# Optimization experiments

Measured on AMD Instinct MI355X. Metric: run time of the kernel, lower is better.

The kernel has to match this reference:

```python
import jax, jax.numpy as jnp
import numpy as np
import math

H = 12   # num_attention_heads
DH = 64  # attention_head_size
D = H * DH  # hidden_size = 768


def _split_heads(x):
    # [b, s, D] -> [b, H, s, DH]
    b, s, _ = x.shape
    return x.reshape(b, s, H, DH).transpose(0, 2, 1, 3)


def setup_inputs() -> dict:
    key = jax.random.key(0)
    ks = jax.random.split(key, 8)
    B, S, G, NUM_CTX = 32, 512, 16, 8
    real_b = B // NUM_CTX
    inp = {
        "hidden_states": jax.random.normal(ks[0], (B, S, D), dtype=jnp.float32),
        "attention_mask": jnp.zeros((B, 1, 1, S), dtype=jnp.float32),
        "global_tokens_embed": jax.random.normal(ks[1], (real_b, G, D), dtype=jnp.float32),
        "Wq": jax.random.normal(ks[2], (D, D), dtype=jnp.float32) * 0.02,
        "bq": jnp.zeros((D,), dtype=jnp.float32),
        "Wk": jax.random.normal(ks[3], (D, D), dtype=jnp.float32) * 0.02,
        "bk": jnp.zeros((D,), dtype=jnp.float32),
        "Wv": jax.random.normal(ks[4], (D, D), dtype=jnp.float32) * 0.02,
        "bv": jnp.zeros((D,), dtype=jnp.float32),
        "num_ctx": 8,
    }
    return inp


def reference(hidden_states, attention_mask, global_tokens_embed,
              Wq, bq, Wk, bk, Wv, bv, num_ctx):
    B, S, _ = hidden_states.shape
    real_b = B // num_ctx
    G = global_tokens_embed.shape[1]
    scale = 1.0 / math.sqrt(DH)

    # Q/K/V projections for packed contexts
    q = _split_heads(hidden_states @ Wq + bq)   # [B,H,S,DH]
    k = _split_heads(hidden_states @ Wk + bk)
    v = _split_heads(hidden_states @ Wv + bv)

    # Global token projections
    gq = _split_heads(global_tokens_embed @ Wq + bq)  # [real_b,H,G,DH]
    gk = _split_heads(global_tokens_embed @ Wk + bk)
    gv = _split_heads(global_tokens_embed @ Wv + bv)

    # ---- Global-token cross attention over all contexts of each real batch ----
    # [B,H,S,DH] -> [real_b, H, num_ctx*S, DH]
    full_k = k.transpose(0, 2, 1, 3).reshape(real_b, num_ctx * S, H, DH).transpose(0, 2, 1, 3)
    full_v = v.transpose(0, 2, 1, 3).reshape(real_b, num_ctx * S, H, DH).transpose(0, 2, 1, 3)
    full_k = jnp.concatenate([gk, full_k], axis=2)  # [real_b,H,G+num_ctx*S,DH]
    full_v = jnp.concatenate([gv, full_v], axis=2)

    g_scores = jnp.einsum('bhgd,bhkd->bhgk', gq, full_k) * scale
    g_mask = attention_mask.reshape(real_b, num_ctx * S)[:, None, None, :]
    g_mask = jnp.concatenate([jnp.zeros((real_b, 1, 1, G), g_mask.dtype), g_mask], axis=3)
    g_scores = g_scores + g_mask
    g_probs = jax.nn.softmax(g_scores, axis=-1)
    g_ctx = jnp.einsum('bhgk,bhkd->bhgd', g_probs, full_v)
    g_ctx = g_ctx.transpose(0, 2, 1, 3).reshape(real_b, G, D)  # [real_b,G,D]

    # ---- Local attention: each context attends to its own tokens + global tokens ----
    gk_rep = jnp.broadcast_to(gk[:, None], (real_b, num_ctx, H, G, DH)).reshape(B, H, G, DH)
    gv_rep = jnp.broadcast_to(gv[:, None], (real_b, num_ctx, H, G, DH)).reshape(B, H, G, DH)
    k2 = jnp.concatenate([gk_rep, k], axis=2)  # [B,H,G+S,DH]
    v2 = jnp.concatenate([gv_rep, v], axis=2)
    mask2 = jnp.concatenate([jnp.zeros((B, 1, 1, G), attention_mask.dtype), attention_mask], axis=3)

    scores = jnp.einsum('bhqd,bhkd->bhqk', q, k2) * scale + mask2  # [B,H,S,G+S]
    probs = jax.nn.softmax(scores, axis=-1)
    ctx = jnp.einsum('bhqk,bhkd->bhqd', probs, v2)
    ctx = ctx.transpose(0, 2, 1, 3).reshape(B, S, D)  # [B,S,D]

    return ctx, g_ctx
```

## Files before the change

### kernel.cpp

```cpp
#include <hip/hip_runtime.h>
#include <hip/hip_bf16.h>
#include <stdint.h>

#define NH 12
#define DHD 64
#define DM 768
#define BB 32
#define SS 512
#define GG 16
#define NCTX 8
#define RBATCH 4
#define OUTG_OFF ((size_t)BB * SS * DM)

#define XROWS 16512
#define NALL 2304
#define NX8 (XROWS * DM / 8)
#define NB8 (NALL / 8)
#define NM8 (BB * SS / 8)

#define LOG2E 1.4426950408889634f
#define QSCALE 0.18033688011112042f

typedef __bf16 bf16x8 __attribute__((ext_vector_type(8)));
typedef float f32x4 __attribute__((ext_vector_type(4)));
typedef float f32x16 __attribute__((ext_vector_type(16)));

__device__ __forceinline__ float b2f(unsigned short u) {
    union { unsigned int i; float f; } x;
    x.i = ((unsigned int)u) << 16;
    return x.f;
}
__device__ __forceinline__ unsigned short f2b(float f) {
    __hip_bfloat16 h = __float2bfloat16(f);
    return *reinterpret_cast<unsigned short*>(&h);
}
__device__ __forceinline__ unsigned int pk2(float a, float b) {
    return ((unsigned int)f2b(b) << 16) | (unsigned int)f2b(a);
}
__device__ __forceinline__ float ex2(float x) {
    return __builtin_amdgcn_exp2f(x);
}
__device__ __forceinline__ float ldv(const void* p, size_t i, int isf32) {
    return isf32 ? ((const float*)p)[i] : b2f(((const unsigned short*)p)[i]);
}
__device__ __forceinline__ void stv(void* p, size_t i, int isf32, float v) {
    if (isf32) ((float*)p)[i] = v;
    else       ((unsigned short*)p)[i] = f2b(v);
}
__device__ __forceinline__ void async_cp16(const unsigned short* g, unsigned short* l) {
    __builtin_amdgcn_global_load_lds(
        (const __attribute__((address_space(1))) unsigned int*)g,
        (__attribute__((address_space(3))) unsigned int*)l, 16, 0, 0);
}

__device__ __forceinline__ void vt_pair_store(unsigned int* Vt32, int vr, int scc,
                                              uint4 a, uint4 b, int ldq) {
    const unsigned int* au = (const unsigned int*)&a;
    const unsigned int* bu = (const unsigned int*)&b;
    #pragma unroll
    for (int i = 0; i < 4; i++) {
        const int d0 = scc + 2 * i;
        const int swz = ((vr >> 3) ^ ((d0 >> 3) & 7));
        const int i32 = d0 * ldq + (swz << 2) + ((vr & 7) >> 1);
        Vt32[i32]       = __builtin_amdgcn_perm(bu[i], au[i], 0x05040100u);
        Vt32[i32 + ldq] = __builtin_amdgcn_perm(bu[i], au[i], 0x07060302u);
    }
}

__global__ __launch_bounds__(256) void detect_dtype(
    const unsigned short* __restrict__ Wq, int* __restrict__ flag)
{
    __shared__ int hi, zz;
    if (threadIdx.x == 0) { hi = 0; zz = 0; }
    __syncthreads();
    int lh = 0, lz = 0;
    for (int i = threadIdx.x; i < 4096; i += 256) {
        unsigned short u = Wq[2 * i];
        if (((u >> 7) & 0xFF) >= 130) lh++;
        if (u == 0) lz++;
    }
    atomicAdd(&hi, lh);
    atomicAdd(&zz, lz);
    __syncthreads();
    if (threadIdx.x == 0) *flag = (hi > 512 || zz > 3500) ? 1 : 0;
}

__global__ __launch_bounds__(256) void cvt_x(
    const void* __restrict__ hs, const void* __restrict__ gte,
    const void* __restrict__ bq, const void* __restrict__ bk,
    const void* __restrict__ bv, const void* __restrict__ mask,
    const int* __restrict__ flag,
    unsigned short* __restrict__ Xb, unsigned short* __restrict__ b_all,
    unsigned short* __restrict__ wmask)
{
    const int e = blockIdx.x * 256 + threadIdx.x;
    const int isf32 = *flag;
    if (e < NX8) {
        const int base = e * 8;
        const int row = base / DM, col = base % DM;
        unsigned short o8[8];
        if (row < 16384) {
            if (isf32) {
                float4 a = ((const float4*)hs)[e * 2];
                float4 c = ((const float4*)hs)[e * 2 + 1];
                o8[0]=f2b(a.x); o8[1]=f2b(a.y); o8[2]=f2b(a.z); o8[3]=f2b(a.w);
                o8[4]=f2b(c.x); o8[5]=f2b(c.y); o8[6]=f2b(c.z); o8[7]=f2b(c.w);
            } else {
                *(uint4*)o8 = ((const uint4*)hs)[e];
            }
        } else if (row < 16448) {
            size_t soff = (size_t)(row - 16384) * DM + col;
            #pragma unroll
            for (int i = 0; i < 8; i++) o8[i] = f2b(ldv(gte, soff + i, isf32));
        } else {
            #pragma unroll
            for (int i = 0; i < 8; i++) o8[i] = 0;
        }
        *(uint4*)&Xb[base] = *(const uint4*)o8;
    } else if (e < NX8 + NB8) {
        const int i0 = (e - NX8) * 8;
        #pragma unroll
        for (int i = 0; i < 8; i++) {
            int ng = i0 + i;
            int z = ng / DM;
            const void* src = (z == 0) ? bq : (z == 1) ? bk : bv;
            b_all[ng] = f2b(ldv(src, ng % DM, isf32));
        }
    } else if (e < NX8 + NB8 + NM8) {
        const int i0 = (e - NX8 - NB8) * 8;
        #pragma unroll
        for (int i = 0; i < 8; i++)
            wmask[i0 + i] = f2b(ldv(mask, i0 + i, isf32) * LOG2E);
    }
}

__global__ __launch_bounds__(256) void cvt_w(
    const void* __restrict__ Wq, const void* __restrict__ Wk,
    const void* __restrict__ Wv, const int* __restrict__ flag,
    unsigned short* __restrict__ Wt)
{
    __shared__ float T[64][65];
    const int kt = blockIdx.x;
    const int ngt = blockIdx.y;
    const int z = ngt / 12, nt = ngt % 12;
    const int tid = threadIdx.x;
    const int isf32 = *flag;
    const void* W = (z == 0) ? Wq : (z == 1) ? Wk : Wv;

    for (int jj = 0; jj < 16; jj++) {
        int el = tid + jj * 256;
        int r = el >> 6, c = el & 63;
        T[r][c] = ldv(W, (size_t)(kt * 64 + r) * DM + nt * 64 + c, isf32);
    }
    __syncthreads();
    for (int jj = 0; jj < 16; jj++) {
        int el = tid + jj * 256;
        int rn = el >> 6, ck = el & 63;
        Wt[(size_t)(z * DM + nt * 64 + rn) * DM + kt * 64 + ck] = f2b(T[ck][rn]);
    }
}

__global__ __launch_bounds__(256) void qkv_gemm(
    const unsigned short* __restrict__ Xb,
    const unsigned short* __restrict__ Wt,
    const unsigned short* __restrict__ b_all,
    unsigned short* __restrict__ q, unsigned short* __restrict__ kk_,
    unsigned short* __restrict__ v,
    unsigned short* __restrict__ gq, unsigned short* __restrict__ gk,
    unsigned short* __restrict__ gv)
{
    __shared__ __align__(16) unsigned short As[128 * 32];
    __shared__ __align__(16) unsigned short Bs[128 * 32];

    const int mt = blockIdx.x, nt = blockIdx.y;
    const int tid = threadIdx.x;
    const int wave = tid >> 6, lane = tid & 63;
    const int quad = lane >> 4, l16 = lane & 15;
    const int wm = wave & 1, wn = wave >> 1;
    const int z = nt / 6;
    unsigned short* YL = (z == 0) ? q : (z == 1) ? kk_ : v;
    unsigned short* YG = (z == 0) ? gq : (z == 1) ? gk : gv;
    const float qsc = (z == 0) ? QSCALE : 1.0f;

    const int sr = tid >> 2, sc = (tid & 3) * 8;

    f32x4 acc[4][4];
    #pragma unroll
    for (int i = 0; i < 4; i++)
        for (int j = 0; j < 4; j++)
            for (int r = 0; r < 4; r++) acc[i][j][r] = 0.f;

    for (int k0 = 0; k0 < DM; k0 += 32) {
        __syncthreads();
        async_cp16(&Xb[(size_t)(mt * 128 + sr) * DM + k0 + sc], &As[wave * 512]);
        async_cp16(&Xb[(size_t)(mt * 128 + 64 + sr) * DM + k0 + sc], &As[2048 + wave * 512]);
        async_cp16(&Wt[(size_t)(nt * 128 + sr) * DM + k0 + sc], &Bs[wave * 512]);
        async_cp16(&Wt[(size_t)(nt * 128 + 64 + sr) * DM + k0 + sc], &Bs[2048 + wave * 512]);
        __syncthreads();

        bf16x8 af[4], bf[4];
        #pragma unroll
        for (int ib = 0; ib < 4; ib++)
            af[ib] = *(const bf16x8*)&As[(wm * 64 + ib * 16 + l16) * 32 + quad * 8];
        #pragma unroll
        for (int jb = 0; jb < 4; jb++)
            bf[jb] = *(const bf16x8*)&Bs[(wn * 64 + jb * 16 + l16) * 32 + quad * 8];
        #pragma unroll
        for (int ib = 0; ib < 4; ib++)
            #pragma unroll
            for (int jb = 0; jb < 4; jb++)
                acc[ib][jb] = __builtin_amdgcn_mfma_f32_16x16x32_bf16(
                    af[ib], bf[jb], acc[ib][jb], 0, 0, 0);
    }

    #pragma unroll
    for (int jb = 0; jb < 4; jb++) {
        const int ng = nt * 128 + wn * 64 + jb * 16 + l16;
        const float bias = b2f(b_all[ng]);
        const int o = ng - z * DM;
        const int h = o >> 6, dh = o & 63;
        #pragma unroll
        for (int ib = 0; ib < 4; ib++) {
            #pragma unroll
            for (int r = 0; r < 4; r++) {
                const int m = mt * 128 + wm * 64 + ib * 16 + quad * 4 + r;
                const unsigned short ob = f2b((acc[ib][jb][r] + bias) * qsc);
                if (m < 16384) {
                    const int b = m >> 9, s = m & 511;
                    YL[(((size_t)b * NH + h) * SS + s) * DHD + dh] = ob;
                } else if (m < 16448) {
                    const int gl = m - 16384;
                    const int rbx = gl >> 4, g = gl & 15;
                    YG[(((size_t)rbx * NH + h) * GG + g) * DHD + dh] = ob;
                }
            }
        }
    }
}

__global__ __launch_bounds__(256) void attn_local(
    const unsigned short* __restrict__ q,
    const unsigned short* __restrict__ k,
    const unsigned short* __restrict__ v,
    const unsigned short* __restrict__ gk,
    const unsigned short* __restrict__ gv,
    const unsigned short* __restrict__ wmask,
    const int* __restrict__ flag,
    void* __restrict__ out)
{
    __shared__ __align__(16) unsigned short Ks[64 * 64];
    __shared__ __align__(16) unsigned short Vt[64 * 64];

    const int qt = blockIdx.x, h = blockIdx.y, b = blockIdx.z;
    const int rb = b >> 3;
    const int tid = threadIdx.x, wave = tid >> 6, lane = tid & 63;
    const int l31 = lane & 31, h8 = lane >> 5;
    const int isf32 = *flag;
    const int q0 = qt * 128 + wave * 32;

    const size_t bh = (size_t)b * NH + h;
    const unsigned short* qp = q + bh * SS * DHD;
    const unsigned short* kp = k + bh * SS * DHD;
    const unsigned short* vp = v + bh * SS * DHD;
    const size_t gbh = (size_t)rb * NH + h;
    const unsigned short* gkp = gk + gbh * GG * DHD;
    const unsigned short* gvp = gv + gbh * GG * DHD;

    bf16x8 qf[4];
    #pragma unroll
    for (int kb = 0; kb < 4; kb++)
        qf[kb] = *(const bf16x8*)&qp[(size_t)(q0 + l31) * DHD + kb * 16 + h8 * 8];

    f32x16 oacc[2];
    #pragma unroll
    for (int mb = 0; mb < 2; mb++)
        #pragma unroll
        for (int j = 0; j < 16; j++) oacc[mb][j] = 0.f;
    float m_s = -1e30f, l_s = 0.f;

    const int sr = tid >> 3, scc = (tid & 7) * 8;
    const int vr = sr * 2;
    const int agc = (((lane & 7) ^ ((lane >> 3) & 7)) << 3);
    const int arow = 8 * wave + (lane >> 3);
    unsigned int* Vt32 = (unsigned int*)Vt;

    for (int t = 0; t < 9; t++) {
        __syncthreads();
        if (t == 0) {
            if (sr < 16) {
                uint4 kx = *(const uint4*)&gkp[sr * DHD + scc];
                *(uint4*)&Ks[sr * 64 + (((scc >> 3) ^ (sr & 7)) << 3)] = kx;
            } else {
                uint4 zz4 = {0, 0, 0, 0};
                *(uint4*)&Ks[sr * 64 + (((scc >> 3) ^ (sr & 7)) << 3)] = zz4;
            }
            uint4 va = {0, 0, 0, 0}, vb = {0, 0, 0, 0};
            if (sr < 8) {
                va = *(const uint4*)&gvp[vr * DHD + scc];
                vb = *(const uint4*)&gvp[(vr + 1) * DHD + scc];
            }
            vt_pair_store(Vt32, vr, scc, va, vb, 32);
        } else {
            const int ks0 = (t - 1) * 64;
            #pragma unroll
            for (int p = 0; p < 2; p++)
                async_cp16(&kp[(size_t)(ks0 + p * 32 + arow) * DHD + agc],
                           &Ks[p * 2048 + wave * 512]);
            uint4 va = *(const uint4*)&vp[(size_t)(ks0 + vr) * DHD + scc];
            uint4 vb = *(const uint4*)&vp[(size_t)(ks0 + vr + 1) * DHD + scc];
            vt_pair_store(Vt32, vr, scc, va, vb, 32);
        }
        __syncthreads();

        f32x16 scA, scB;
        #pragma unroll
        for (int kt = 0; kt < 2; kt++) {
            f32x16 cc;
            #pragma unroll
            for (int j = 0; j < 16; j++) cc[j] = 0.f;
            if (kt == 0 || t > 0) {
                #pragma unroll
                for (int kb = 0; kb < 4; kb++) {
                    const int key = kt * 32 + l31;
                    bf16x8 kf = *(const bf16x8*)&Ks[key * 64 + (((kb * 2 + h8) ^ (key & 7)) << 3)];
                    cc = __builtin_amdgcn_mfma_f32_32x32x16_bf16(kf, qf[kb], cc, 0, 0, 0);
                }
                if (t > 0) {
                    #pragma unroll
                    for (int rg = 0; rg < 4; rg++) {
                        uint2 mu = *(const uint2*)&wmask[b * SS + (t - 1) * 64 + kt * 32 + rg * 8 + 4 * h8];
                        const unsigned short* mp = (const unsigned short*)&mu;
                        #pragma unroll
                        for (int r = 0; r < 4; r++)
                            cc[rg * 4 + r] += b2f(mp[r]);
                    }
                } else {
                    #pragma unroll
                    for (int j = 8; j < 16; j++) cc[j] = -1e30f;
                }
            } else {
                #pragma unroll
                for (int j = 0; j < 16; j++) cc[j] = -1e30f;
            }
            if (kt == 0) scA = cc; else scB = cc;
        }

        float mx = -1e30f;
        #pragma unroll
        for (int j = 0; j < 16; j++) mx = fmaxf(mx, scA[j]);
        #pragma unroll
        for (int j = 0; j < 16; j++) mx = fmaxf(mx, scB[j]);
        mx = fmaxf(mx, __shfl_xor(mx, 32, 64));
        if (!__all(mx <= m_s)) {
            const float mn = fmaxf(m_s, mx);
            const float alpha = ex2(m_s - mn);
            m_s = mn;
            l_s *= alpha;
            #pragma unroll
            for (int mb = 0; mb < 2; mb++)
                #pragma unroll
                for (int j = 0; j < 16; j++) oacc[mb][j] *= alpha;
        }
        float rs = 0.f;
        #pragma unroll
        for (int j = 0; j < 16; j++) { float pw = ex2(scA[j] - m_s); scA[j] = pw; rs += pw; }
        #pragma unroll
        for (int j = 0; j < 16; j++) { float pw = ex2(scB[j] - m_s); scB[j] = pw; rs += pw; }
        rs += __shfl_xor(rs, 32, 64);
        l_s += rs;

        #pragma unroll
        for (int kt = 0; kt < 2; kt++) {
            unsigned int wA[4], wB[4];
            #pragma unroll
            for (int g = 0; g < 4; g++) {
                const float s0 = (kt == 0) ? scA[4 * g + 0] : scB[4 * g + 0];
                const float s1 = (kt == 0) ? scA[4 * g + 1] : scB[4 * g + 1];
                const float s2 = (kt == 0) ? scA[4 * g + 2] : scB[4 * g + 2];
                const float s3 = (kt == 0) ? scA[4 * g + 3] : scB[4 * g + 3];
                wA[g] = pk2(s0, s1);
                wB[g] = pk2(s2, s3);
            }
            #pragma unroll
            for (int kb = 0; kb < 2; kb++) {
                auto ra  = __builtin_amdgcn_permlane32_swap(wA[2 * kb], wA[2 * kb + 1], false, false);
                auto rbp = __builtin_amdgcn_permlane32_swap(wB[2 * kb], wB[2 * kb + 1], false, false);
                union { unsigned int u[4]; bf16x8 v8; } pfu;
                pfu.u[0] = (unsigned int)ra[0];
                pfu.u[1] = (unsigned int)rbp[0];
                pfu.u[2] = (unsigned int)ra[1];
                pfu.u[3] = (unsigned int)rbp[1];
                const int kb2 = kt * 2 + kb;
                #pragma unroll
                for (int mb = 0; mb < 2; mb++) {
                    const int d = mb * 32 + l31;
                    bf16x8 vf = *(const bf16x8*)&Vt[d * 64 + (((kb2 * 2 + h8) ^ ((d >> 3) & 7)) << 3)];
                    oacc[mb] = __builtin_amdgcn_mfma_f32_32x32x16_bf16(vf, pfu.v8, oacc[mb], 0, 0, 0);
                }
            }
        }
    }

    const float inv = 1.f / l_s;
    const int s = q0 + l31;
    #pragma unroll
    for (int mb = 0; mb < 2; mb++) {
        #pragma unroll
        for (int rg = 0; rg < 4; rg++) {
            const int d0 = mb * 32 + rg * 8 + 4 * h8;
            const size_t idx = ((size_t)b * SS + s) * DM + h * DHD + d0;
            if (isf32) {
                float4 o4;
                o4.x = oacc[mb][rg * 4 + 0] * inv;
                o4.y = oacc[mb][rg * 4 + 1] * inv;
                o4.z = oacc[mb][rg * 4 + 2] * inv;
                o4.w = oacc[mb][rg * 4 + 3] * inv;
                *(float4*)&((float*)out)[idx] = o4;
            } else {
                uint2 o2;
                o2.x = pk2(oacc[mb][rg * 4 + 0] * inv, oacc[mb][rg * 4 + 1] * inv);
                o2.y = pk2(oacc[mb][rg * 4 + 2] * inv, oacc[mb][rg * 4 + 3] * inv);
                *(uint2*)&((unsigned short*)out)[idx] = o2;
            }
        }
    }
}

__global__ __launch_bounds__(256) void attn_gsplit(
    const unsigned short* __restrict__ k,
    const unsigned short* __restrict__ v,
    const unsigned short* __restrict__ gq,
    const unsigned short* __restrict__ gk,
    const unsigned short* __restrict__ gv,
    const unsigned short* __restrict__ wmask,
    float* __restrict__ Opart, float* __restrict__ Mpart,
    float* __restrict__ Lpart)
{
    __shared__ __align__(16) unsigned short Ks[128 * 64];
    __shared__ __align__(16) unsigned short Vt[64 * 128];
    __shared__ __align__(16) unsigned short Ps[4 * 16 * 64];

    const int h = blockIdx.x, rb = blockIdx.y, sp = blockIdx.z;
    const int tid = threadIdx.x, wave = tid >> 6, lane = tid & 63;
    const int quad = lane >> 4, l16 = lane & 15;

    const size_t gbh = (size_t)rb * NH + h;
    const unsigned short* gqp = gq + gbh * GG * DHD;
    const unsigned short* gkp = gk + gbh * GG * DHD;
    const unsigned short* gvp = gv + gbh * GG * DHD;

    bf16x8 aq[2];
    aq[0] = *(const bf16x8*)&gqp[l16 * DHD + quad * 8];
    aq[1] = *(const bf16x8*)&gqp[l16 * DHD + 32 + quad * 8];

    f32x4 oacc[4];
    #pragma unroll
    for (int db = 0; db < 4; db++)
        for (int r = 0; r < 4; r++) oacc[db][r] = 0.f;
    float m_s = -1e30f, l_s = 0.f;

    const int sr = tid >> 3, scc = (tid & 7) * 8;
    const int vr = sr * 2;
    const int agc = (((lane & 7) ^ ((lane >> 3) & 7)) << 3);
    const int arow = 8 * wave + (lane >> 3);
    unsigned short* myP = &Ps[wave * 1024];
    unsigned int* Vt32 = (unsigned int*)Vt;

    const int nt = (sp == 0) ? 9 : 8;
    for (int ti = 0; ti < nt; ti++) {
        const bool gtile = (sp == 0 && ti == 0);
        int cb = 0, soff = 0;
        __syncthreads();
        if (gtile) {
            if (sr < 16) {
                uint4 kx = *(const uint4*)&gkp[sr * DHD + scc];
                *(uint4*)&Ks[sr * 64 + (((scc >> 3) ^ (sr & 7)) << 3)] = kx;
                uint4 va = {0, 0, 0, 0}, vb = {0, 0, 0, 0};
                if (sr < 8) {
                    va = *(const uint4*)&gvp[vr * DHD + scc];
                    vb = *(const uint4*)&gvp[(vr + 1) * DHD + scc];
                }
                vt_pair_store(Vt32, vr, scc, va, vb, 64);
            } else {
                uint4 zz4 = {0, 0, 0, 0};
                *(uint4*)&Ks[sr * 64 + (((scc >> 3) ^ (sr & 7)) << 3)] = zz4;
            }
        } else {
            const int kidx = sp * 1024 + (ti - ((sp == 0) ? 1 : 0)) * 128;
            cb = rb * NCTX + (kidx >> 9);
            soff = kidx & 511;
            const unsigned short* kp = k + ((size_t)cb * NH + h) * SS * DHD;
            const unsigned short* vp = v + ((size_t)cb * NH + h) * SS * DHD;
            #pragma unroll
            for (int p = 0; p < 4; p++)
                async_cp16(&kp[(size_t)(soff + p * 32 + arow) * DHD + agc],
                           &Ks[p * 2048 + wave * 512]);
            #pragma unroll
            for (int pp = 0; pp < 2; pp++) {
                const int vrr = vr + pp * 64;
                uint4 va = *(const uint4*)&vp[(size_t)(soff + vrr) * DHD + scc];
                uint4 vb = *(const uint4*)&vp[(size_t)(soff + vrr + 1) * DHD + scc];
                vt_pair_store(Vt32, vrr, scc, va, vb, 64);
            }
        }
        __syncthreads();

        if (gtile && wave != 0) continue;

        const int nbn = gtile ? 1 : 2;
        f32x4 c[2];
        for (int hh = 0; hh < nbn; hh++) {
            f32x4 cc = {0.f, 0.f, 0.f, 0.f};
            const int key = wave * 32 + hh * 16 + l16;
            #pragma unroll
            for (int kd = 0; kd < 2; kd++) {
                bf16x8 kf = *(const bf16x8*)&Ks[key * 64 + (((kd * 4 + quad) ^ (key & 7)) << 3)];
                cc = __builtin_amdgcn_mfma_f32_16x16x32_bf16(kf, aq[kd], cc, 0, 0, 0);
            }
            if (!gtile) {
                uint2 mu = *(const uint2*)&wmask[cb * SS + soff + wave * 32 + hh * 16 + quad * 4];
                const unsigned short* mp = (const unsigned short*)&mu;
                #pragma unroll
                for (int r = 0; r < 4; r++)
                    cc[r] += b2f(mp[r]);
            }
            c[hh] = cc;
        }

        float mx = -1e30f;
        for (int hh = 0; hh < nbn; hh++)
            #pragma unroll
            for (int r = 0; r < 4; r++) mx = fmaxf(mx, c[hh][r]);
        mx = fmaxf(mx, __shfl_xor(mx, 16, 64));
        mx = fmaxf(mx, __shfl_xor(mx, 32, 64));
        const float mn = fmaxf(m_s, mx);
        const float alpha = ex2(m_s - mn);
        m_s = mn;
        float rs = 0.f;
        for (int hh = 0; hh < nbn; hh++)
            #pragma unroll
            for (int r = 0; r < 4; r++) {
                float p = ex2(c[hh][r] - mn);
                c[hh][r] = p;
                rs += p;
            }
        rs += __shfl_xor(rs, 16, 64);
        rs += __shfl_xor(rs, 32, 64);
        l_s = l_s * alpha + rs;
        #pragma unroll
        for (int db = 0; db < 4; db++)
            for (int r = 0; r < 4; r++) oacc[db][r] *= alpha;

        for (int hh = 0; hh < nbn; hh++) {
            uint2 pw;
            pw.x = pk2(c[hh][0], c[hh][1]);
            pw.y = pk2(c[hh][2], c[hh][3]);
            const int cch = ((hh * 2 + (quad >> 1)) ^ (l16 & 7));
            *(uint2*)&myP[l16 * 64 + cch * 8 + (quad & 1) * 4] = pw;
        }
        if (nbn == 1) {
            uint2 zz2; zz2.x = 0; zz2.y = 0;
            const int cch = ((2 + (quad >> 1)) ^ (l16 & 7));
            *(uint2*)&myP[l16 * 64 + cch * 8 + (quad & 1) * 4] = zz2;
        }

        bf16x8 pf = *(const bf16x8*)&myP[l16 * 64 + ((quad ^ (l16 & 7)) << 3)];
        #pragma unroll
        for (int db = 0; db < 4; db++) {
            const int d = db * 16 + l16;
            const int kc = wave * 4 + quad;
            bf16x8 vf = *(const bf16x8*)&Vt[d * 128 + ((kc ^ ((d >> 3) & 7)) << 3)];
            oacc[db] = __builtin_amdgcn_mfma_f32_16x16x32_bf16(vf, pf, oacc[db], 0, 0, 0);
        }
    }

    __syncthreads();
    float* Om = (float*)Ks;
    float* Mw = (float*)Vt;
    float* Lw = Mw + 64;
    #pragma unroll
    for (int db = 0; db < 4; db++)
        for (int r = 0; r < 4; r++)
            Om[(wave * 16 + l16) * 64 + db * 16 + quad * 4 + r] = oacc[db][r];
    if (quad == 0) {
        Mw[wave * 16 + l16] = m_s;
        Lw[wave * 16 + l16] = l_s;
    }
    __syncthreads();

    const size_t pbase = ((size_t)(sp * RBATCH + rb) * NH + h) * 1024;
    for (int e = tid; e < 1024; e += 256) {
        const int qrow = e >> 6, d = e & 63;
        float M = fmaxf(fmaxf(Mw[qrow], Mw[16 + qrow]), fmaxf(Mw[32 + qrow], Mw[48 + qrow]));
        float acc = 0.f, L = 0.f;
        #pragma unroll
        for (int w = 0; w < 4; w++) {
            float scw = ex2(Mw[w * 16 + qrow] - M);
            acc += Om[(w * 16 + qrow) * 64 + d] * scw;
            L += Lw[w * 16 + qrow] * scw;
        }
        Opart[pbase + e] = acc;
        if (d == 0) {
            Mpart[((sp * RBATCH + rb) * NH + h) * 16 + qrow] = M;
            Lpart[((sp * RBATCH + rb) * NH + h) * 16 + qrow] = L;
        }
    }
}

__global__ __launch_bounds__(256) void attn_gmerge(
    const float* __restrict__ Opart, const float* __restrict__ Mpart,
    const float* __restrict__ Lpart, const int* __restrict__ flag,
    void* __restrict__ out)
{
    const int h = blockIdx.x, rb = blockIdx.y;
    const int tid = threadIdx.x;
    const int isf32 = *flag;
    for (int e = tid; e < 1024; e += 256) {
        const int qrow = e >> 6, d = e & 63;
        float M = -1e30f;
        #pragma unroll
        for (int sp = 0; sp < 4; sp++)
            M = fmaxf(M, Mpart[((sp * RBATCH + rb) * NH + h) * 16 + qrow]);
        float acc = 0.f, L = 0.f;
        #pragma unroll
        for (int sp = 0; sp < 4; sp++) {
            const size_t pb = ((size_t)(sp * RBATCH + rb) * NH + h);
            float scs = ex2(Mpart[pb * 16 + qrow] - M);
            acc += Opart[pb * 1024 + e] * scs;
            L += Lpart[pb * 16 + qrow] * scs;
        }
        stv(out, OUTG_OFF + ((size_t)rb * GG + qrow) * DM + h * DHD + d, isf32, acc / L);
    }
}

extern "C" void kernel_launch(void* const* d_in, const int* in_sizes, int n_in,
                              void* d_out, int out_size, void* d_ws, size_t ws_size,
                              hipStream_t stream) {
    const void* hs   = d_in[0];
    const void* mask = d_in[1];
    const void* gte  = d_in[2];
    const void* Wq   = d_in[3];
    const void* bq   = d_in[4];
    const void* Wk   = d_in[5];
    const void* bk   = d_in[6];
    const void* Wv   = d_in[7];
    const void* bv   = d_in[8];

    const size_t qkv_sz = (size_t)BB * NH * SS * DHD;
    const size_t g_sz   = (size_t)RBATCH * NH * GG * DHD;
    const size_t msk_sz = (size_t)BB * SS;
    const size_t x_sz   = (size_t)XROWS * DM;
    const size_t wt_sz  = (size_t)NALL * DM;
    const size_t ba_sz  = (size_t)NALL;
    const size_t need_hw = 3 * qkv_sz + 3 * g_sz + msk_sz + x_sz + wt_sz + ba_sz;
    if (ws_size < need_hw * 2 + 16) return;

    unsigned short* q     = (unsigned short*)d_ws;
    unsigned short* kk    = q + qkv_sz;
    unsigned short* vv    = kk + qkv_sz;
    unsigned short* gq    = vv + qkv_sz;
    unsigned short* gk    = gq + g_sz;
    unsigned short* gv    = gk + g_sz;
    unsigned short* wmask = gv + g_sz;
    unsigned short* Xb    = wmask + msk_sz;
    unsigned short* Wt    = Xb + x_sz;
    unsigned short* b_all = Wt + wt_sz;
    int* flag = (int*)(b_all + ba_sz);
    float* Opart = (float*)Xb;
    float* Mpart = Opart + 4 * RBATCH * NH * 1024;
    float* Lpart = Mpart + 4 * RBATCH * NH * 16;

    detect_dtype<<<1, 256, 0, stream>>>((const unsigned short*)Wq, flag);

    const int cvt_items = NX8 + NB8 + NM8;
    cvt_x<<<(cvt_items + 255) / 256, 256, 0, stream>>>(
        hs, gte, bq, bk, bv, mask, flag, Xb, b_all, wmask);
    cvt_w<<<dim3(12, 36), 256, 0, stream>>>(Wq, Wk, Wv, flag, Wt);

    qkv_gemm<<<dim3(129, 18), 256, 0, stream>>>(Xb, Wt, b_all, q, kk, vv, gq, gk, gv);

    attn_local<<<dim3(4, NH, BB), 256, 0, stream>>>(
        q, kk, vv, gk, gv, wmask, flag, d_out);
    attn_gsplit<<<dim3(NH, RBATCH, 4), 256, 0, stream>>>(
        kk, vv, gq, gk, gv, wmask, Opart, Mpart, Lpart);
    attn_gmerge<<<dim3(NH, RBATCH), 256, 0, stream>>>(
        Opart, Mpart, Lpart, flag, d_out);
}
```

Before: 360.5 us.

## Double-buffer QKV GEMM, swizzle blocks across XCDs, vectorize epilogue stores

The QKV GEMM now double-buffers its LDS tiles, so the async copies for the next K-slice are issued while MFMAs run on the current one, and it needs one barrier per iteration instead of two. Both the GEMM and the local attention kernel switch to 1D grids whose block IDs are remapped so that consecutive tiles land on the same XCD, which should improve L2 reuse of shared X and W rows. The GEMM swaps its MFMA operands so each lane holds four consecutive output columns, which lets the epilogue use 8-byte packed stores with vector bias loads instead of scalar 2-byte stores. In exchange LDS use doubles, and the swizzle assumes round-robin dispatch across 8 XCDs.

Measured after the change: 345.1 us. -4.3%, faster.

```diff
diff --git a/kernel.cpp b/kernel.cpp
--- a/kernel.cpp
+++ b/kernel.cpp
@@ -160,6 +160,7 @@
     }
 }
 
+#define QKV_NWG (129 * 18)
 __global__ __launch_bounds__(256) void qkv_gemm(
     const unsigned short* __restrict__ Xb,
     const unsigned short* __restrict__ Wt,
@@ -169,10 +170,15 @@
     unsigned short* __restrict__ gq, unsigned short* __restrict__ gk,
     unsigned short* __restrict__ gv)
 {
-    __shared__ __align__(16) unsigned short As[128 * 32];
-    __shared__ __align__(16) unsigned short Bs[128 * 32];
-
-    const int mt = blockIdx.x, nt = blockIdx.y;
+    __shared__ __align__(16) unsigned short As[2][128 * 32];
+    __shared__ __align__(16) unsigned short Bs[2][128 * 32];
+
+    const int orig = blockIdx.x;
+    const int q8 = QKV_NWG >> 3, r8 = QKV_NWG & 7;
+    const int xcd = orig & 7, lin = orig >> 3;
+    const int swz = (xcd < r8 ? xcd * (q8 + 1) : r8 * (q8 + 1) + (xcd - r8) * q8) + lin;
+    const int mt = swz / 18, nt = swz - mt * 18;
+
     const int tid = threadIdx.x;
     const int wave = tid >> 6, lane = tid & 63;
     const int quad = lane >> 4, l16 = lane & 15;
@@ -184,60 +190,83 @@
 
     const int sr = tid >> 2, sc = (tid & 3) * 8;
 
+    const unsigned short* Arow0 = &Xb[(size_t)(mt * 128 + sr) * DM + sc];
+    const unsigned short* Arow1 = Arow0 + (size_t)64 * DM;
+    const unsigned short* Brow0 = &Wt[(size_t)(nt * 128 + sr) * DM + sc];
+    const unsigned short* Brow1 = Brow0 + (size_t)64 * DM;
+
     f32x4 acc[4][4];
     #pragma unroll
     for (int i = 0; i < 4; i++)
         for (int j = 0; j < 4; j++)
             for (int r = 0; r < 4; r++) acc[i][j][r] = 0.f;
 
-    for (int k0 = 0; k0 < DM; k0 += 32) {
-        __syncthreads();
-        async_cp16(&Xb[(size_t)(mt * 128 + sr) * DM + k0 + sc], &As[wave * 512]);
-        async_cp16(&Xb[(size_t)(mt * 128 + 64 + sr) * DM + k0 + sc], &As[2048 + wave * 512]);
-        async_cp16(&Wt[(size_t)(nt * 128 + sr) * DM + k0 + sc], &Bs[wave * 512]);
-        async_cp16(&Wt[(size_t)(nt * 128 + 64 + sr) * DM + k0 + sc], &Bs[2048 + wave * 512]);
-        __syncthreads();
+    async_cp16(Arow0, &As[0][wave * 512]);
+    async_cp16(Arow1, &As[0][2048 + wave * 512]);
+    async_cp16(Brow0, &Bs[0][wave * 512]);
+    async_cp16(Brow1, &Bs[0][2048 + wave * 512]);
+    __syncthreads();
+
+    int cur = 0;
+    for (int t = 0; t < 24; t++) {
+        if (t < 23) {
+            const int kn = (t + 1) * 32;
+            async_cp16(Arow0 + kn, &As[cur ^ 1][wave * 512]);
+            async_cp16(Arow1 + kn, &As[cur ^ 1][2048 + wave * 512]);
+            async_cp16(Brow0 + kn, &Bs[cur ^ 1][wave * 512]);
+            async_cp16(Brow1 + kn, &Bs[cur ^ 1][2048 + wave * 512]);
+        }
 
         bf16x8 af[4], bf[4];
         #pragma unroll
         for (int ib = 0; ib < 4; ib++)
-            af[ib] = *(const bf16x8*)&As[(wm * 64 + ib * 16 + l16) * 32 + quad * 8];
+            af[ib] = *(const bf16x8*)&As[cur][(wm * 64 + ib * 16 + l16) * 32 + quad * 8];
         #pragma unroll
         for (int jb = 0; jb < 4; jb++)
-            bf[jb] = *(const bf16x8*)&Bs[(wn * 64 + jb * 16 + l16) * 32 + quad * 8];
+            bf[jb] = *(const bf16x8*)&Bs[cur][(wn * 64 + jb * 16 + l16) * 32 + quad * 8];
         #pragma unroll
         for (int ib = 0; ib < 4; ib++)
             #pragma unroll
             for (int jb = 0; jb < 4; jb++)
                 acc[ib][jb] = __builtin_amdgcn_mfma_f32_16x16x32_bf16(
-                    af[ib], bf[jb], acc[ib][jb], 0, 0, 0);
+                    bf[jb], af[ib], acc[ib][jb], 0, 0, 0);
+
+        if (t < 23) __syncthreads();
+        cur ^= 1;
     }
 
     #pragma unroll
-    for (int jb = 0; jb < 4; jb++) {
-        const int ng = nt * 128 + wn * 64 + jb * 16 + l16;
-        const float bias = b2f(b_all[ng]);
-        const int o = ng - z * DM;
-        const int h = o >> 6, dh = o & 63;
-        #pragma unroll
-        for (int ib = 0; ib < 4; ib++) {
-            #pragma unroll
-            for (int r = 0; r < 4; r++) {
-                const int m = mt * 128 + wm * 64 + ib * 16 + quad * 4 + r;
-                const unsigned short ob = f2b((acc[ib][jb][r] + bias) * qsc);
-                if (m < 16384) {
-                    const int b = m >> 9, s = m & 511;
-                    YL[(((size_t)b * NH + h) * SS + s) * DHD + dh] = ob;
-                } else if (m < 16448) {
-                    const int gl = m - 16384;
-                    const int rbx = gl >> 4, g = gl & 15;
-                    YG[(((size_t)rbx * NH + h) * GG + g) * DHD + dh] = ob;
-                }
-            }
-        }
-    }
-}
-
+    for (int ib = 0; ib < 4; ib++) {
+        const int m = mt * 128 + wm * 64 + ib * 16 + l16;
+        if (m >= 16448) continue;
+        const bool loc = (m < 16384);
+        const int b = m >> 9, s = m & 511;
+        const int gl = m - 16384;
+        const int rbx = gl >> 4, g = gl & 15;
+        #pragma unroll
+        for (int jb = 0; jb < 4; jb++) {
+            const int ng0 = nt * 128 + wn * 64 + jb * 16 + quad * 4;
+            const int o = ng0 - z * DM;
+            const int h = o >> 6, dh0 = o & 63;
+            const uint2 bu = *(const uint2*)&b_all[ng0];
+            const unsigned short* bp = (const unsigned short*)&bu;
+            const float y0 = (acc[ib][jb][0] + b2f(bp[0])) * qsc;
+            const float y1 = (acc[ib][jb][1] + b2f(bp[1])) * qsc;
+            const float y2 = (acc[ib][jb][2] + b2f(bp[2])) * qsc;
+            const float y3 = (acc[ib][jb][3] + b2f(bp[3])) * qsc;
+            uint2 o2;
+            o2.x = pk2(y0, y1);
+            o2.y = pk2(y2, y3);
+            if (loc) {
+                *(uint2*)&YL[(((size_t)b * NH + h) * SS + s) * DHD + dh0] = o2;
+            } else {
+                *(uint2*)&YG[(((size_t)rbx * NH + h) * GG + g) * DHD + dh0] = o2;
+            }
+        }
+    }
+}
+
+#define AL_NWG (4 * NH * BB)
 __global__ __launch_bounds__(256) void attn_local(
     const unsigned short* __restrict__ q,
     const unsigned short* __restrict__ k,
@@ -251,7 +280,12 @@
     __shared__ __align__(16) unsigned short Ks[64 * 64];
     __shared__ __align__(16) unsigned short Vt[64 * 64];
 
-    const int qt = blockIdx.x, h = blockIdx.y, b = blockIdx.z;
+    const int orig = blockIdx.x;
+    const int swz = (orig & 7) * (AL_NWG / 8) + (orig >> 3);
+    const int qt = swz & 3;
+    const int hb = swz >> 2;
+    const int h = hb % NH, b = hb / NH;
+
     const int rb = b >> 3;
     const int tid = threadIdx.x, wave = tid >> 6, lane = tid & 63;
     const int l31 = lane & 31, h8 = lane >> 5;
@@ -677,9 +711,9 @@
         hs, gte, bq, bk, bv, mask, flag, Xb, b_all, wmask);
     cvt_w<<<dim3(12, 36), 256, 0, stream>>>(Wq, Wk, Wv, flag, Wt);
 
-    qkv_gemm<<<dim3(129, 18), 256, 0, stream>>>(Xb, Wt, b_all, q, kk, vv, gq, gk, gv);
-
-    attn_local<<<dim3(4, NH, BB), 256, 0, stream>>>(
+    qkv_gemm<<<dim3(QKV_NWG), 256, 0, stream>>>(Xb, Wt, b_all, q, kk, vv, gq, gk, gv);
+
+    attn_local<<<dim3(AL_NWG), 256, 0, stream>>>(
         q, kk, vv, gk, gv, wmask, flag, d_out);
     attn_gsplit<<<dim3(NH, RBATCH, 4), 256, 0, stream>>>(
         kk, vv, gq, gk, gv, wmask, Opart, Mpart, Lpart);
```
